# Performance work log

Hardware: AMD Instinct MI355X
Metric: run time of the kernel (lower is better)

## Reference

```python
import jax, jax.numpy as jnp
import numpy as np

E = 8        # n_routed_experts
K = 4        # num_experts_per_tok
T = 1024     # tokens
H = 1024     # hidden_size
I = 1408     # moe_intermediate_size


def setup_inputs() -> dict:
    key = jax.random.key(0)
    ks = jax.random.split(key, 6)
    hidden_states = jax.random.normal(ks[0], (T, H), jnp.float32)
    rw = jax.random.uniform(ks[1], (T, K), jnp.float32)
    router_weights = rw / jnp.sum(rw, axis=-1, keepdims=True)  # normalized top-k router weights
    selected_experts = jax.random.randint(ks[2], (T, K), 0, E, jnp.int32)
    gate_w = jax.random.normal(ks[3], (E, H, I), jnp.float32) * (H ** -0.5)  # lecun_normal-ish
    up_w = jax.random.normal(ks[4], (E, H, I), jnp.float32) * (H ** -0.5)
    down_w = jax.random.normal(ks[5], (E, I, H), jnp.float32) * (I ** -0.5)
    return {
        'hidden_states': hidden_states,
        'router_weights': router_weights,
        'gate_w': gate_w,
        'up_w': up_w,
        'down_w': down_w,
        'selected_experts': selected_experts,
    }


def _grouped_matmul(x, w, seg):
    # x: [m, k] tokens sorted by expert; w: [E, k, n]; seg: [m] expert id per row.
    # Grouped GEMM expressed as E masked GEMMs (fixed small loop over experts);
    # a custom kernel would do true variable-group-size grouped GEMM.
    out = jnp.zeros((x.shape[0], w.shape[-1]), x.dtype)
    for e in range(w.shape[0]):
        out = out + jnp.where((seg == e)[:, None], x, jnp.zeros((), x.dtype)) @ w[e]
    return out


def reference(hidden_states, router_weights, gate_w, up_w, down_w, selected_experts):
    t, k = selected_experts.shape
    flat = selected_experts.ravel()                       # [t*k]
    hs = jnp.repeat(hidden_states, k, axis=0)             # [t*k, H]
    sort_idx = jnp.argsort(flat)                          # dispatch: sort tokens by expert
    seg = flat[sort_idx]
    xs = hs[sort_idx]
    gate = _grouped_matmul(xs, gate_w, seg)               # [t*k, I]
    up = _grouped_matmul(xs, up_w, seg)                   # [t*k, I]
    h = jax.nn.silu(gate) * up                            # fused SwiGLU
    down = _grouped_matmul(h, down_w, seg)                # [t*k, H]
    unsort = jnp.argsort(sort_idx)                        # scatter back to token order
    out = down[unsort].reshape(t, k, -1)
    return jnp.sum(out * router_weights[..., None], axis=1)  # weighted combine [t, H]
```

## Files before the change

### kernel.cpp

```cpp
#include <hip/hip_runtime.h>
#include <hip/hip_bf16.h>
#include <cstdint>
#include <cstddef>

#define NE 8
#define NT 1024
#define NK 4
#define NH 1024
#define NI 1408
#define NA (NT * NK)
#define BM 128
#define MAXTILES 40
#define PADSLOTS 5120

typedef short short8 __attribute__((ext_vector_type(8)));
typedef float f32x4 __attribute__((ext_vector_type(4)));
typedef unsigned short u16;

#define WS_HDR   0
#define WS_SORT  1024
#define WS_XBF   21504
#define WS_GT    2118656
#define WS_UT    25187328
#define WS_DT    48256000
#define WS_HB    71324672
#define WS_DTMP  85742592

__device__ __forceinline__ u16 f2b(float f) {
  union { float f; uint32_t u; } c; c.f = f;
  uint32_t u = c.u;
  return (u16)((u + 0x7FFFu + ((u >> 16) & 1u)) >> 16);
}

__device__ __forceinline__ void llds16(const void* g, void* l) {
  __builtin_amdgcn_global_load_lds(
      (const __attribute__((address_space(1))) void*)g,
      (__attribute__((address_space(3))) void*)l, 16, 0, 0);
}

__global__ void bucket_kernel(const int* __restrict__ sel, int* __restrict__ hdr,
                              int* __restrict__ sorted) {
  __shared__ int cnt[NE], fill[NE], poff_s[NE + 1];
  int tid = threadIdx.x;
  if (tid < NE) { cnt[tid] = 0; fill[tid] = 0; }
  __syncthreads();
  for (int i = tid; i < NA; i += 256) atomicAdd(&cnt[sel[i]], 1);
  __syncthreads();
  if (tid == 0) {
    int off = 0, nt = 0;
    for (int e = 0; e < NE; ++e) {
      poff_s[e] = off;
      int tiles = (cnt[e] + BM - 1) / BM;
      for (int j = 0; j < tiles; ++j) { hdr[32 + nt] = e; hdr[80 + nt] = off + j * BM; ++nt; }
      off += tiles * BM;
    }
    poff_s[NE] = off;
    hdr[17] = nt;
    for (int e = 0; e < NE; ++e) hdr[e] = cnt[e];
    for (int e = 0; e <= NE; ++e) hdr[8 + e] = poff_s[e];
  }
  __syncthreads();
  for (int i = tid; i < PADSLOTS; i += 256) sorted[i] = -1;
  __syncthreads();
  for (int i = tid; i < NA; i += 256) {
    int e = sel[i];
    int p = atomicAdd(&fill[e], 1);
    sorted[poff_s[e] + p] = i;
  }
}

__global__ void cvt_x_kernel(const float* __restrict__ src, u16* __restrict__ dst) {
  int i = (blockIdx.x * 256 + threadIdx.x) * 4;
  float4 v = *(const float4*)&src[i];
  ushort4 o;
  o.x = f2b(v.x); o.y = f2b(v.y); o.z = f2b(v.z); o.w = f2b(v.w);
  *(ushort4*)&dst[i] = o;
}

__global__ void transcvt_kernel(const float* __restrict__ src, u16* __restrict__ dst,
                                int K, int N) {
  __shared__ float t[32][33];
  int e = blockIdx.z;
  int n0 = blockIdx.x * 32, k0 = blockIdx.y * 32;
  int tx = threadIdx.x & 31, ty = threadIdx.x >> 5;
  const float* s = src + (size_t)e * K * N;
  u16* d = dst + (size_t)e * K * N;
  for (int j = 0; j < 4; ++j)
    t[ty + 8 * j][tx] = s[(size_t)(k0 + ty + 8 * j) * N + n0 + tx];
  __syncthreads();
  for (int j = 0; j < 4; ++j)
    d[(size_t)(n0 + ty + 8 * j) * K + k0 + tx] = f2b(t[tx][ty + 8 * j]);
}

__global__ __launch_bounds__(256, 2) void gemm1_kernel(
    const u16* __restrict__ xbf, const u16* __restrict__ gT, const u16* __restrict__ uT,
    u16* __restrict__ hbuf, const int* __restrict__ hdr, const int* __restrict__ sorted) {
  int tile = blockIdx.x;
  if (tile >= hdr[17]) return;
  int e = hdr[32 + tile];
  int slot0 = hdr[80 + tile];
  int n0 = blockIdx.y * 64;
  int tid = threadIdx.x;

  __shared__ u16 sA[128 * 64];
  __shared__ u16 sBg[64 * 64];
  __shared__ u16 sBu[64 * 64];

  const u16* aptr[4];
  for (int s = 0; s < 4; ++s) {
    int idx = s * 256 + tid;
    int row = idx >> 3, kc = idx & 7;
    int as = sorted[slot0 + row];
    int trow = (as >= 0) ? (as >> 2) : 0;
    aptr[s] = xbf + (size_t)trow * NH + kc * 8;
  }
  const u16 *bgp[2], *bup[2];
  for (int s = 0; s < 2; ++s) {
    int idx = s * 256 + tid;
    int n = idx >> 3, kc = idx & 7;
    size_t o = ((size_t)e * NI + n0 + n) * NH + kc * 8;
    bgp[s] = gT + o; bup[s] = uT + o;
  }

  int lane = tid & 63, wave = tid >> 6;
  int wm = wave >> 1, wn = wave & 1;
  int l15 = lane & 15, quad = lane >> 4;

  f32x4 accg[4][2] = {}; f32x4 accu[4][2] = {};

  for (int kt = 0; kt < NH / 64; ++kt) {
    int ko = kt * 64;
    for (int s = 0; s < 4; ++s) llds16(aptr[s] + ko, &sA[(s * 256 + tid) * 8]);
    for (int s = 0; s < 2; ++s) {
      llds16(bgp[s] + ko, &sBg[(s * 256 + tid) * 8]);
      llds16(bup[s] + ko, &sBu[(s * 256 + tid) * 8]);
    }
    __syncthreads();
    for (int ks = 0; ks < 2; ++ks) {
      short8 av[4], bg[2], bu[2];
      for (int mf = 0; mf < 4; ++mf)
        av[mf] = *(const short8*)&sA[(wm * 64 + mf * 16 + l15) * 64 + ks * 32 + quad * 8];
      for (int nf = 0; nf < 2; ++nf) {
        bg[nf] = *(const short8*)&sBg[(wn * 32 + nf * 16 + l15) * 64 + ks * 32 + quad * 8];
        bu[nf] = *(const short8*)&sBu[(wn * 32 + nf * 16 + l15) * 64 + ks * 32 + quad * 8];
      }
      for (int mf = 0; mf < 4; ++mf)
        for (int nf = 0; nf < 2; ++nf) {
          accg[mf][nf] = __builtin_amdgcn_mfma_f32_16x16x32_bf16(av[mf], bg[nf], accg[mf][nf], 0, 0, 0);
          accu[mf][nf] = __builtin_amdgcn_mfma_f32_16x16x32_bf16(av[mf], bu[nf], accu[mf][nf], 0, 0, 0);
        }
    }
    __syncthreads();
  }

  for (int mf = 0; mf < 4; ++mf)
    for (int nf = 0; nf < 2; ++nf)
      for (int r = 0; r < 4; ++r) {
        int row = wm * 64 + mf * 16 + quad * 4 + r;
        int col = n0 + wn * 32 + nf * 16 + l15;
        float g = accg[mf][nf][r], u = accu[mf][nf][r];
        float hv = (g / (1.f + __expf(-g))) * u;
        hbuf[(size_t)(slot0 + row) * NI + col] = f2b(hv);
      }
}

__global__ __launch_bounds__(256, 2) void gemm2_kernel(
    const u16* __restrict__ hbuf, const u16* __restrict__ dT,
    float* __restrict__ dtmp, const int* __restrict__ hdr, const int* __restrict__ sorted) {
  int tile = blockIdx.x;
  if (tile >= hdr[17]) return;
  int e = hdr[32 + tile];
  int slot0 = hdr[80 + tile];
  int n0 = blockIdx.y * 128;
  int tid = threadIdx.x;

  __shared__ u16 sA[128 * 64];
  __shared__ u16 sB[128 * 64];

  const u16 *ap[4], *bp[4];
  for (int s = 0; s < 4; ++s) {
    int idx = s * 256 + tid;
    int r = idx >> 3, kc = idx & 7;
    ap[s] = hbuf + (size_t)(slot0 + r) * NI + kc * 8;
    bp[s] = dT + ((size_t)e * NH + n0 + r) * NI + kc * 8;
  }

  int lane = tid & 63, wave = tid >> 6;
  int wm = wave >> 1, wn = wave & 1;
  int l15 = lane & 15, quad = lane >> 4;

  f32x4 acc[4][4] = {};

  for (int kt = 0; kt < NI / 64; ++kt) {
    int ko = kt * 64;
    for (int s = 0; s < 4; ++s) llds16(ap[s] + ko, &sA[(s * 256 + tid) * 8]);
    for (int s = 0; s < 4; ++s) llds16(bp[s] + ko, &sB[(s * 256 + tid) * 8]);
    __syncthreads();
    for (int ks = 0; ks < 2; ++ks) {
      short8 av[4], bv[4];
      for (int mf = 0; mf < 4; ++mf)
        av[mf] = *(const short8*)&sA[(wm * 64 + mf * 16 + l15) * 64 + ks * 32 + quad * 8];
      for (int nf = 0; nf < 4; ++nf)
        bv[nf] = *(const short8*)&sB[(wn * 64 + nf * 16 + l15) * 64 + ks * 32 + quad * 8];
      for (int mf = 0; mf < 4; ++mf)
        for (int nf = 0; nf < 4; ++nf)
          acc[mf][nf] = __builtin_amdgcn_mfma_f32_16x16x32_bf16(av[mf], bv[nf], acc[mf][nf], 0, 0, 0);
    }
    __syncthreads();
  }

  for (int mf = 0; mf < 4; ++mf) {
    int rowb = wm * 64 + mf * 16 + quad * 4;
    for (int r = 0; r < 4; ++r) {
      int as = sorted[slot0 + rowb + r];
      if (as < 0) continue;
      float* orow = dtmp + (size_t)as * NH + n0 + wn * 64;
      for (int nf = 0; nf < 4; ++nf)
        orow[nf * 16 + l15] = acc[mf][nf][r];
    }
  }
}

__global__ void combine_kernel(const float* __restrict__ dtmp, const float* __restrict__ rw,
                               float* __restrict__ out) {
  int t = blockIdx.x;
  int c = threadIdx.x * 4;
  float4 acc = make_float4(0.f, 0.f, 0.f, 0.f);
  for (int k = 0; k < NK; ++k) {
    float w = rw[t * NK + k];
    float4 v = *(const float4*)&dtmp[(size_t)(t * NK + k) * NH + c];
    acc.x += w * v.x; acc.y += w * v.y; acc.z += w * v.z; acc.w += w * v.w;
  }
  *(float4*)&out[(size_t)t * NH + c] = acc;
}

extern "C" void kernel_launch(void* const* d_in, const int* in_sizes, int n_in,
                              void* d_out, int out_size, void* d_ws, size_t ws_size,
                              hipStream_t stream) {
  const float* hs  = (const float*)d_in[0];
  const float* rw  = (const float*)d_in[1];
  const float* gw  = (const float*)d_in[2];
  const float* uw  = (const float*)d_in[3];
  const float* dw  = (const float*)d_in[4];
  const int*   sel = (const int*)d_in[5];
  float* out = (float*)d_out;

  char* ws = (char*)d_ws;
  int*  hdr    = (int*)(ws + WS_HDR);
  int*  sorted = (int*)(ws + WS_SORT);
  u16*  xbf    = (u16*)(ws + WS_XBF);
  u16*  gT     = (u16*)(ws + WS_GT);
  u16*  uT     = (u16*)(ws + WS_UT);
  u16*  dT     = (u16*)(ws + WS_DT);
  u16*  hb     = (u16*)(ws + WS_HB);
  float* dtmp  = (float*)(ws + WS_DTMP);

  hipLaunchKernelGGL(bucket_kernel, dim3(1), dim3(256), 0, stream, sel, hdr, sorted);
  hipLaunchKernelGGL(cvt_x_kernel, dim3(NT * NH / 1024), dim3(256), 0, stream, hs, xbf);
  hipLaunchKernelGGL(transcvt_kernel, dim3(NI / 32, NH / 32, NE), dim3(256), 0, stream, gw, gT, NH, NI);
  hipLaunchKernelGGL(transcvt_kernel, dim3(NI / 32, NH / 32, NE), dim3(256), 0, stream, uw, uT, NH, NI);
  hipLaunchKernelGGL(transcvt_kernel, dim3(NH / 32, NI / 32, NE), dim3(256), 0, stream, dw, dT, NI, NH);
  hipLaunchKernelGGL(gemm1_kernel, dim3(MAXTILES, NI / 64), dim3(256), 0, stream, xbf, gT, uT, hb, hdr, sorted);
  hipLaunchKernelGGL(gemm2_kernel, dim3(MAXTILES, NH / 128), dim3(256), 0, stream, hb, dT, dtmp, hdr, sorted);
  hipLaunchKernelGGL(combine_kernel, dim3(NT), dim3(256), 0, stream, dtmp, rw, out);
}
```

Baseline: 282.8 us.

## Merge weight transpose kernels with vectorized I/O and XOR-swizzle GEMM LDS tiles

Replaces three per-tensor 32x32 transpose-convert launches with one 64x64-tile kernel that handles all three weight tensors, using float4 loads and 16-byte bf16 stores. Separately, the GEMM kernels now XOR-swizzle the 16-byte k-chunk position by row when filling LDS and apply the same swizzle on fragment reads. The swizzle is meant to remove LDS bank conflicts during MFMA operand loads. The larger transpose tile raises LDS use per block, and the rows read from t[kc*8+j][n] may still hit some bank conflicts.

```diff
diff --git a/kernel.cpp b/kernel.cpp
--- a/kernel.cpp
+++ b/kernel.cpp
@@ -77,19 +77,36 @@
   *(ushort4*)&dst[i] = o;
 }
 
-__global__ void transcvt_kernel(const float* __restrict__ src, u16* __restrict__ dst,
-                                int K, int N) {
-  __shared__ float t[32][33];
-  int e = blockIdx.z;
-  int n0 = blockIdx.x * 32, k0 = blockIdx.y * 32;
-  int tx = threadIdx.x & 31, ty = threadIdx.x >> 5;
-  const float* s = src + (size_t)e * K * N;
-  u16* d = dst + (size_t)e * K * N;
-  for (int j = 0; j < 4; ++j)
-    t[ty + 8 * j][tx] = s[(size_t)(k0 + ty + 8 * j) * N + n0 + tx];
-  __syncthreads();
-  for (int j = 0; j < 4; ++j)
-    d[(size_t)(n0 + ty + 8 * j) * K + k0 + tx] = f2b(t[tx][ty + 8 * j]);
+__global__ __launch_bounds__(256) void transcvt_all(
+    const float* __restrict__ gw, const float* __restrict__ uw, const float* __restrict__ dw,
+    u16* __restrict__ gT, u16* __restrict__ uT, u16* __restrict__ dT) {
+  __shared__ float t[64][65];
+  int z = blockIdx.z;
+  int tensor = z >> 3, e = z & 7;
+  const float* src; u16* dst; int K, N, kb, nb;
+  if (tensor == 0)      { src = gw; dst = gT; }
+  else if (tensor == 1) { src = uw; dst = uT; }
+  else                  { src = dw; dst = dT; }
+  if (tensor < 2) { K = NH; N = NI; nb = blockIdx.x; kb = blockIdx.y; }
+  else            { K = NI; N = NH; kb = blockIdx.x; nb = blockIdx.y; }
+  int k0 = kb * 64, n0 = nb * 64;
+  src += (size_t)e * K * N;
+  dst += (size_t)e * K * N;
+  int tid = threadIdx.x;
+  for (int i = 0; i < 4; ++i) {
+    int idx = i * 256 + tid;
+    int r = idx >> 4, c = idx & 15;
+    *(float4*)&t[r][c * 4] = *(const float4*)&src[(size_t)(k0 + r) * N + n0 + c * 4];
+  }
+  __syncthreads();
+  for (int i = 0; i < 2; ++i) {
+    int idx = i * 256 + tid;
+    int n = idx >> 3, kc = idx & 7;
+    u16 o[8];
+#pragma unroll
+    for (int j = 0; j < 8; ++j) o[j] = f2b(t[kc * 8 + j][n]);
+    *(short8*)&dst[(size_t)(n0 + n) * K + k0 + kc * 8] = *(const short8*)o;
+  }
 }
 
 __global__ __launch_bounds__(256, 2) void gemm1_kernel(
@@ -109,7 +126,8 @@
   const u16* aptr[4];
   for (int s = 0; s < 4; ++s) {
     int idx = s * 256 + tid;
-    int row = idx >> 3, kc = idx & 7;
+    int row = idx >> 3, c = idx & 7;
+    int kc = c ^ (row & 7);
     int as = sorted[slot0 + row];
     int trow = (as >= 0) ? (as >> 2) : 0;
     aptr[s] = xbf + (size_t)trow * NH + kc * 8;
@@ -117,7 +135,8 @@
   const u16 *bgp[2], *bup[2];
   for (int s = 0; s < 2; ++s) {
     int idx = s * 256 + tid;
-    int n = idx >> 3, kc = idx & 7;
+    int n = idx >> 3, c = idx & 7;
+    int kc = c ^ (n & 7);
     size_t o = ((size_t)e * NI + n0 + n) * NH + kc * 8;
     bgp[s] = gT + o; bup[s] = uT + o;
   }
@@ -125,6 +144,7 @@
   int lane = tid & 63, wave = tid >> 6;
   int wm = wave >> 1, wn = wave & 1;
   int l15 = lane & 15, quad = lane >> 4;
+  int sw = l15 & 7;
 
   f32x4 accg[4][2] = {}; f32x4 accu[4][2] = {};
 
@@ -137,12 +157,13 @@
     }
     __syncthreads();
     for (int ks = 0; ks < 2; ++ks) {
+      int pos = ((ks * 4 + quad) ^ sw) * 8;
       short8 av[4], bg[2], bu[2];
       for (int mf = 0; mf < 4; ++mf)
-        av[mf] = *(const short8*)&sA[(wm * 64 + mf * 16 + l15) * 64 + ks * 32 + quad * 8];
+        av[mf] = *(const short8*)&sA[(wm * 64 + mf * 16 + l15) * 64 + pos];
       for (int nf = 0; nf < 2; ++nf) {
-        bg[nf] = *(const short8*)&sBg[(wn * 32 + nf * 16 + l15) * 64 + ks * 32 + quad * 8];
-        bu[nf] = *(const short8*)&sBu[(wn * 32 + nf * 16 + l15) * 64 + ks * 32 + quad * 8];
+        bg[nf] = *(const short8*)&sBg[(wn * 32 + nf * 16 + l15) * 64 + pos];
+        bu[nf] = *(const short8*)&sBu[(wn * 32 + nf * 16 + l15) * 64 + pos];
       }
       for (int mf = 0; mf < 4; ++mf)
         for (int nf = 0; nf < 2; ++nf) {
@@ -180,7 +201,8 @@
   const u16 *ap[4], *bp[4];
   for (int s = 0; s < 4; ++s) {
     int idx = s * 256 + tid;
-    int r = idx >> 3, kc = idx & 7;
+    int r = idx >> 3, c = idx & 7;
+    int kc = c ^ (r & 7);
     ap[s] = hbuf + (size_t)(slot0 + r) * NI + kc * 8;
     bp[s] = dT + ((size_t)e * NH + n0 + r) * NI + kc * 8;
   }
@@ -188,6 +210,7 @@
   int lane = tid & 63, wave = tid >> 6;
   int wm = wave >> 1, wn = wave & 1;
   int l15 = lane & 15, quad = lane >> 4;
+  int sw = l15 & 7;
 
   f32x4 acc[4][4] = {};
 
@@ -197,11 +220,12 @@
     for (int s = 0; s < 4; ++s) llds16(bp[s] + ko, &sB[(s * 256 + tid) * 8]);
     __syncthreads();
     for (int ks = 0; ks < 2; ++ks) {
+      int pos = ((ks * 4 + quad) ^ sw) * 8;
       short8 av[4], bv[4];
       for (int mf = 0; mf < 4; ++mf)
-        av[mf] = *(const short8*)&sA[(wm * 64 + mf * 16 + l15) * 64 + ks * 32 + quad * 8];
+        av[mf] = *(const short8*)&sA[(wm * 64 + mf * 16 + l15) * 64 + pos];
       for (int nf = 0; nf < 4; ++nf)
-        bv[nf] = *(const short8*)&sB[(wn * 64 + nf * 16 + l15) * 64 + ks * 32 + quad * 8];
+        bv[nf] = *(const short8*)&sB[(wn * 64 + nf * 16 + l15) * 64 + pos];
       for (int mf = 0; mf < 4; ++mf)
         for (int nf = 0; nf < 4; ++nf)
           acc[mf][nf] = __builtin_amdgcn_mfma_f32_16x16x32_bf16(av[mf], bv[nf], acc[mf][nf], 0, 0, 0);
@@ -257,9 +281,7 @@
 
   hipLaunchKernelGGL(bucket_kernel, dim3(1), dim3(256), 0, stream, sel, hdr, sorted);
   hipLaunchKernelGGL(cvt_x_kernel, dim3(NT * NH / 1024), dim3(256), 0, stream, hs, xbf);
-  hipLaunchKernelGGL(transcvt_kernel, dim3(NI / 32, NH / 32, NE), dim3(256), 0, stream, gw, gT, NH, NI);
-  hipLaunchKernelGGL(transcvt_kernel, dim3(NI / 32, NH / 32, NE), dim3(256), 0, stream, uw, uT, NH, NI);
-  hipLaunchKernelGGL(transcvt_kernel, dim3(NH / 32, NI / 32, NE), dim3(256), 0, stream, dw, dT, NI, NH);
+  hipLaunchKernelGGL(transcvt_all, dim3(22, 16, 24), dim3(256), 0, stream, gw, uw, dw, gT, uT, dT);
   hipLaunchKernelGGL(gemm1_kernel, dim3(MAXTILES, NI / 64), dim3(256), 0, stream, xbf, gT, uT, hb, hdr, sorted);
   hipLaunchKernelGGL(gemm2_kernel, dim3(MAXTILES, NH / 128), dim3(256), 0, stream, hb, dT, dtmp, hdr, sorted);
   hipLaunchKernelGGL(combine_kernel, dim3(NT), dim3(256), 0, stream, dtmp, rw, out);
```

Measured after the change: 261.0 us. -7.7%, faster.
